# Kernel tuning notes

Hardware: AMD Instinct MI355X
Metric: run time of the kernel (lower is better)

Reference implementation:

```python
import jax, jax.numpy as jnp
import numpy as np

B, S, E, H, I = 32, 257, 1024, 16, 4096
D = E // H  # head_dim = 64
EPS = 1e-5


def setup_inputs() -> dict:
    key = jax.random.key(0)
    ks = jax.random.split(key, 12)
    std = 0.02
    inp = {
        'hidden_states': jax.random.normal(ks[0], (B, S, E), jnp.float32),
        'attention_mask': jnp.zeros((B, 1, S, S), jnp.float32),
        'causal_attention_mask': jnp.zeros((B, 1, S, S), jnp.float32),
        'ln1_w': jnp.ones((E,), jnp.float32),
        'ln1_b': jnp.zeros((E,), jnp.float32),
        'q_w': jax.random.normal(ks[1], (E, E), jnp.float32) * std,
        'q_b': jnp.zeros((E,), jnp.float32),
        'k_w': jax.random.normal(ks[2], (E, E), jnp.float32) * std,
        'k_b': jnp.zeros((E,), jnp.float32),
        'v_w': jax.random.normal(ks[3], (E, E), jnp.float32) * std,
        'v_b': jnp.zeros((E,), jnp.float32),
        'o_w': jax.random.normal(ks[4], (E, E), jnp.float32) * std,
        'o_b': jnp.zeros((E,), jnp.float32),
        'ln2_w': jnp.ones((E,), jnp.float32),
        'ln2_b': jnp.zeros((E,), jnp.float32),
        'fc1_w': jax.random.normal(ks[5], (I, E), jnp.float32) * std,
        'fc1_b': jnp.zeros((I,), jnp.float32),
        'fc2_w': jax.random.normal(ks[6], (E, I), jnp.float32) * std,
        'fc2_b': jnp.zeros((E,), jnp.float32),
    }
    return inp


def _layernorm(x, w, b):
    mu = jnp.mean(x, axis=-1, keepdims=True)
    var = jnp.mean(jnp.square(x - mu), axis=-1, keepdims=True)
    return (x - mu) * jax.lax.rsqrt(var + EPS) * w + b


def _gelu_tanh(x):
    # 0.5*x*(1+tanh(sqrt(2/pi)*(x+0.044715*x^3)))
    c = np.sqrt(2.0 / np.pi).astype(np.float32)
    return 0.5 * x * (1.0 + jnp.tanh(c * (x + 0.044715 * x * x * x)))


def reference(hidden_states, attention_mask, causal_attention_mask,
              ln1_w, ln1_b, q_w, q_b, k_w, k_b, v_w, v_b, o_w, o_b,
              ln2_w, ln2_b, fc1_w, fc1_b, fc2_w, fc2_b):
    scale = D ** -0.5
    residual = hidden_states
    x = _layernorm(hidden_states, ln1_w, ln1_b)

    # projections (torch Linear: x @ W.T + b), q pre-scaled as in source
    q = (x @ q_w.T + q_b) * scale
    k = x @ k_w.T + k_b
    v = x @ v_w.T + v_b

    # [B, H, S, D]
    q = q.reshape(B, S, H, D).transpose(0, 2, 1, 3)
    k = k.reshape(B, S, H, D).transpose(0, 2, 1, 3)
    v = v.reshape(B, S, H, D).transpose(0, 2, 1, 3)

    scores = jnp.einsum('bhqd,bhkd->bhqk', q, k)  # [B,H,S,S]
    scores = scores + causal_attention_mask + attention_mask
    probs = jax.nn.softmax(scores, axis=-1)
    ctx = jnp.einsum('bhqk,bhkd->bhqd', probs, v)
    ctx = ctx.transpose(0, 2, 1, 3).reshape(B, S, E)
    attn_out = ctx @ o_w.T + o_b

    h = residual + attn_out
    residual = h
    x = _layernorm(h, ln2_w, ln2_b)
    x = _gelu_tanh(x @ fc1_w.T + fc1_b)
    x = x @ fc2_w.T + fc2_b
    return residual + x
```

## Files before the change

### kernel.cpp

```cpp
#include <hip/hip_runtime.h>

typedef unsigned short u16;
typedef unsigned int   u32;
typedef short s16x8 __attribute__((ext_vector_type(8)));
typedef float f32x4 __attribute__((ext_vector_type(4)));

#define MFMA16(A,B,C) __builtin_amdgcn_mfma_f32_16x16x32_bf16((A),(B),(C),0,0,0)
#define BAR()  asm volatile("s_barrier" ::: "memory")
#define VMC4   asm volatile("s_waitcnt vmcnt(4)" ::: "memory")
#define VMC0   asm volatile("s_waitcnt vmcnt(0)" ::: "memory")

#define B_   32
#define S_   257
#define E_   1024
#define H_   16
#define D_   64
#define I_   4096
#define M_   (B_*S_)

__device__ __forceinline__ u16 f2bf(float f) {
    u32 u = __float_as_uint(f);
    u32 r = u + 0x7fffu + ((u >> 16) & 1u);
    return (u16)(r >> 16);
}
__device__ __forceinline__ float bf2f(u16 b) {
    return __uint_as_float(((u32)b) << 16);
}

__device__ __forceinline__ void gload16(const void* g, void* l) {
    __builtin_amdgcn_global_load_lds(
        (const __attribute__((address_space(1))) u32*)g,
        (__attribute__((address_space(3))) u32*)l, 16, 0, 0);
}

__global__ __launch_bounds__(256)
void convert_w_kernel(const float* __restrict__ qw, const float* __restrict__ kw,
                      const float* __restrict__ vw, const float* __restrict__ ow,
                      const float* __restrict__ f1, const float* __restrict__ f2,
                      u16* __restrict__ dst)
{
    const int total4 = (12 * 1048576) / 4;
    for (int i = blockIdx.x * 256 + threadIdx.x; i < total4; i += gridDim.x * 256) {
        int e = i * 4;
        int seg = e >> 20;
        const float* srcp; int off;
        if (seg < 4)      { srcp = (seg == 0 ? qw : seg == 1 ? kw : seg == 2 ? vw : ow); off = e & 1048575; }
        else if (seg < 8) { srcp = f1; off = e - 4 * 1048576; }
        else              { srcp = f2; off = e - 8 * 1048576; }
        float4 v = *(const float4*)(srcp + off);
        ushort4 o;
        o.x = f2bf(v.x); o.y = f2bf(v.y); o.z = f2bf(v.z); o.w = f2bf(v.w);
        *(ushort4*)(dst + e) = o;
    }
}

__global__ __launch_bounds__(256)
void mask_combine_kernel(const float* __restrict__ am, const float* __restrict__ cm,
                         u16* __restrict__ msum)
{
    const int total = B_ * S_ * 272;
    for (int i = blockIdx.x * 256 + threadIdx.x; i < total; i += gridDim.x * 256) {
        int skv = i % 272;
        int rem = i / 272;
        int sq  = rem % S_;
        int b   = rem / S_;
        float v;
        if (skv < S_) {
            size_t o = ((size_t)b * S_ + sq) * S_ + skv;
            v = am[o] + cm[o];
        } else v = -1e30f;
        msum[i] = f2bf(v);
    }
}

__global__ __launch_bounds__(256)
void ln_kernel(const float* __restrict__ src, const float* __restrict__ gam,
               const float* __restrict__ bet, u16* __restrict__ dst)
{
    int row = blockIdx.x;
    const float4* p = (const float4*)(src + (size_t)row * E_);
    float4 x = p[threadIdx.x];
    float s  = x.x + x.y + x.z + x.w;
    float s2 = x.x * x.x + x.y * x.y + x.z * x.z + x.w * x.w;
#pragma unroll
    for (int xm = 1; xm < 64; xm <<= 1) {
        s  += __shfl_xor(s,  xm, 64);
        s2 += __shfl_xor(s2, xm, 64);
    }
    __shared__ float red[8];
    int wv = threadIdx.x >> 6;
    if ((threadIdx.x & 63) == 0) { red[wv] = s; red[4 + wv] = s2; }
    __syncthreads();
    s  = red[0] + red[1] + red[2] + red[3];
    s2 = red[4] + red[5] + red[6] + red[7];
    float mu  = s * (1.0f / 1024.0f);
    float var = s2 * (1.0f / 1024.0f) - mu * mu;
    float rs  = rsqrtf(var + 1e-5f);
    float4 g  = ((const float4*)gam)[threadIdx.x];
    float4 be = ((const float4*)bet)[threadIdx.x];
    ushort4 o;
    o.x = f2bf((x.x - mu) * rs * g.x + be.x);
    o.y = f2bf((x.y - mu) * rs * g.y + be.y);
    o.z = f2bf((x.z - mu) * rs * g.z + be.z);
    o.w = f2bf((x.w - mu) * rs * g.w + be.w);
    ((ushort4*)dst)[(size_t)row * 256 + threadIdx.x] = o;
}

template<int MODE>
__global__ __launch_bounds__(256, 3)
void gemm4(const u16* __restrict__ A,
           const u16* __restrict__ Bq, const u16* __restrict__ Bk, const u16* __restrict__ Bv,
           const float* __restrict__ biasq, const float* __restrict__ biask, const float* __restrict__ biasvv,
           const float* __restrict__ res, float* __restrict__ outF,
           u16* __restrict__ outBq, u16* __restrict__ outBk, u16* __restrict__ outBv,
           int M, int N, int K)
{
    __shared__ u16 lds[2][2][4096];
    const int tid = threadIdx.x, lane = tid & 63, w = tid >> 6;
    const int lr = lane & 15, lg = lane >> 4;
    const int wm = w >> 1, wn = w & 1;

    const u16* Bm = Bq; const float* bias = biasq; u16* outB = outBq;
    float scl = 1.0f;
    int nt = blockIdx.y;
    if (MODE == 0) {
        int mat = nt >> 3; nt &= 7;
        if (mat == 1)      { Bm = Bk; bias = biask; outB = outBk; }
        else if (mat == 2) { Bm = Bv; bias = biasvv; outB = outBv; }
        if (mat == 0) scl = 0.125f;
    }
    const int m0 = blockIdx.x * 128, n0 = nt * 128;
    const int NTt = K >> 5;

    const int p    = tid * 16;
    const int l_   = p ^ (((p >> 7) & 3) << 4);
    const int srow = l_ >> 6;
    const int scol = (l_ & 63) >> 1;
    const int wbase = w * 1024;

    auto STAGE = [&](int buf, int t) {
        const int kc = t << 5;
        {   int gr = m0 + srow;       if (gr > M - 1) gr = M - 1;
            gload16(A  + (size_t)gr * K + kc + scol, (char*)&lds[buf][0][0] + wbase); }
        {   int gr = m0 + 64 + srow;  if (gr > M - 1) gr = M - 1;
            gload16(A  + (size_t)gr * K + kc + scol, (char*)&lds[buf][0][0] + 4096 + wbase); }
        {   int gr = n0 + srow;       if (gr > N - 1) gr = N - 1;
            gload16(Bm + (size_t)gr * K + kc + scol, (char*)&lds[buf][1][0] + wbase); }
        {   int gr = n0 + 64 + srow;  if (gr > N - 1) gr = N - 1;
            gload16(Bm + (size_t)gr * K + kc + scol, (char*)&lds[buf][1][0] + 4096 + wbase); }
    };
    auto LDA = [&](int buf, int mf) -> s16x8 {
        const char* b = (const char*)&lds[buf][0][0];
        int row = wm * 64 + mf * 16 + lr;
        return *(const s16x8*)(b + row * 64 + ((lg * 16) ^ (((row >> 1) & 3) << 4)));
    };
    auto LDB = [&](int buf, int nf) -> s16x8 {
        const char* b = (const char*)&lds[buf][1][0];
        int row = wn * 64 + nf * 16 + lr;
        return *(const s16x8*)(b + row * 64 + ((lg * 16) ^ (((row >> 1) & 3) << 4)));
    };

    f32x4 acc[4][4];
#pragma unroll
    for (int i = 0; i < 4; ++i)
#pragma unroll
        for (int j = 0; j < 4; ++j) { f32x4 z = {0.f, 0.f, 0.f, 0.f}; acc[i][j] = z; }

    STAGE(0, 0);
    STAGE(1, 1);
    VMC4;
    BAR();

    for (int t = 0; t < NTt; ++t) {
        const int cur = t & 1;
        s16x8 bf[4], af[4];
#pragma unroll
        for (int nf = 0; nf < 4; ++nf) bf[nf] = LDB(cur, nf);
#pragma unroll
        for (int mf = 0; mf < 4; ++mf) af[mf] = LDA(cur, mf);
#pragma unroll
        for (int mf = 0; mf < 4; ++mf)
#pragma unroll
            for (int nf = 0; nf < 4; ++nf)
                acc[mf][nf] = MFMA16(af[mf], bf[nf], acc[mf][nf]);
        BAR();
        if (t + 2 < NTt) STAGE(cur, t + 2);
        if (t + 1 < NTt) {
            if (t + 2 < NTt) { VMC4; } else { VMC0; }
        }
        BAR();
    }

    float biasv[4];
#pragma unroll
    for (int nf = 0; nf < 4; ++nf)
        biasv[nf] = bias[n0 + wn * 64 + nf * 16 + lr];

#pragma unroll
    for (int mf = 0; mf < 4; ++mf) {
#pragma unroll
        for (int r = 0; r < 4; ++r) {
            int row = m0 + wm * 64 + mf * 16 + lg * 4 + r;
            if (row >= M) continue;
            if (MODE == 0) {
                int bb = row / S_;
                int ss = row - bb * S_;
#pragma unroll
                for (int nf = 0; nf < 4; ++nf) {
                    int col = n0 + wn * 64 + nf * 16 + lr;
                    int hh = col >> 6, dd = col & 63;
                    float v = (acc[mf][nf][r] + biasv[nf]) * scl;
                    outB[(((size_t)bb * H_ + hh) * S_ + ss) * D_ + dd] = f2bf(v);
                }
            } else if (MODE == 1) {
                size_t base = (size_t)row * N;
#pragma unroll
                for (int nf = 0; nf < 4; ++nf) {
                    int col = n0 + wn * 64 + nf * 16 + lr;
                    outF[base + col] = acc[mf][nf][r] + biasv[nf] + res[base + col];
                }
            } else {
                size_t base = (size_t)row * N;
#pragma unroll
                for (int nf = 0; nf < 4; ++nf) {
                    int col = n0 + wn * 64 + nf * 16 + lr;
                    float x = acc[mf][nf][r] + biasv[nf];
                    float u2 = 1.5957691216057308f * (x + 0.044715f * x * x * x);
                    u2 = fminf(u2, 80.0f);
                    float tt = __expf(u2);
                    outB[base + col] = f2bf(x * tt / (1.0f + tt));
                }
            }
        }
    }
}

__global__ __launch_bounds__(256)
void attn_kernel(const u16* __restrict__ qg_, const u16* __restrict__ kg_,
                 const u16* __restrict__ vg_, const u16* __restrict__ msum,
                 u16* __restrict__ ctx)
{
    __shared__ u16 Ks[272 * 72];
    __shared__ u16 Vt[64 * 296];
    __shared__ u16 Ps[4][16 * 32];
    const int bh = blockIdx.x;
    const int b = bh >> 4, hh = bh & 15;
    const u16* kg = kg_ + (size_t)bh * (S_ * D_);
    const u16* vg = vg_ + (size_t)bh * (S_ * D_);
    const u16* qg = qg_ + (size_t)bh * (S_ * D_);
    const int tid = threadIdx.x, lane = tid & 63, wv = tid >> 6;

    for (int c = tid; c < (S_ * D_) / 8; c += 256) {
        int s = c >> 3, d8 = (c & 7) << 3;
        s16x8 val = *(const s16x8*)(kg + s * 64 + d8);
        *(s16x8*)&Ks[s * 72 + d8] = val;
    }
    for (int idx = tid; idx < 15 * 64; idx += 256) {
        int rr = 257 + (idx >> 6), cc = idx & 63;
        Ks[rr * 72 + cc] = 0;
    }
    for (int c = tid; c < (S_ * D_) / 8; c += 256) {
        int s = c >> 3, d8 = (c & 7) << 3;
        s16x8 val = *(const s16x8*)(vg + s * 64 + d8);
#pragma unroll
        for (int j = 0; j < 8; ++j) Vt[(d8 + j) * 296 + s] = (u16)val[j];
    }
    for (int idx = tid; idx < 64 * 39; idx += 256) {
        int dd = idx / 39, cc = 257 + idx % 39;
        Vt[dd * 296 + cc] = 0;
    }
    __syncthreads();

    const int lr = lane & 15, lg = lane >> 4;
    for (int qb = wv; qb < 17; qb += 4) {
        const int q0 = qb * 16;
        int qrow = q0 + lr; if (qrow > S_ - 1) qrow = S_ - 1;
        s16x8 aq0 = *(const s16x8*)(qg + qrow * 64 + lg * 8);
        s16x8 aq1 = *(const s16x8*)(qg + qrow * 64 + 32 + lg * 8);

        f32x4 sc[17];
#pragma unroll
        for (int t = 0; t < 17; ++t) { f32x4 z = {0.f, 0.f, 0.f, 0.f}; sc[t] = z; }
#pragma unroll
        for (int t = 0; t < 17; ++t) {
            s16x8 b0 = *(const s16x8*)&Ks[(t * 16 + lr) * 72 + lg * 8];
            s16x8 b1 = *(const s16x8*)&Ks[(t * 16 + lr) * 72 + 32 + lg * 8];
            sc[t] = MFMA16(aq0, b0, sc[t]);
            sc[t] = MFMA16(aq1, b1, sc[t]);
        }
        float mx[4] = {-3e38f, -3e38f, -3e38f, -3e38f};
#pragma unroll
        for (int r = 0; r < 4; ++r) {
            int sq = q0 + lg * 4 + r; if (sq > S_ - 1) sq = S_ - 1;
            const u16* mrow = msum + ((size_t)b * S_ + sq) * 272;
#pragma unroll
            for (int t = 0; t < 17; ++t) {
                sc[t][r] += bf2f(mrow[t * 16 + lr]);
                mx[r] = fmaxf(mx[r], sc[t][r]);
            }
        }
#pragma unroll
        for (int r = 0; r < 4; ++r) {
#pragma unroll
            for (int xm = 1; xm <= 8; xm <<= 1)
                mx[r] = fmaxf(mx[r], __shfl_xor(mx[r], xm, 64));
        }
        float sum[4] = {0.f, 0.f, 0.f, 0.f};
#pragma unroll
        for (int t = 0; t < 17; ++t)
#pragma unroll
            for (int r = 0; r < 4; ++r) {
                float e = __expf(sc[t][r] - mx[r]);
                sc[t][r] = e; sum[r] += e;
            }
#pragma unroll
        for (int r = 0; r < 4; ++r) {
#pragma unroll
            for (int xm = 1; xm <= 8; xm <<= 1)
                sum[r] += __shfl_xor(sum[r], xm, 64);
        }

        f32x4 ac[4];
#pragma unroll
        for (int nt = 0; nt < 4; ++nt) { f32x4 z = {0.f, 0.f, 0.f, 0.f}; ac[nt] = z; }
        u16* myP = &Ps[wv][0];
#pragma unroll
        for (int kc = 0; kc < 9; ++kc) {
#pragma unroll
            for (int tt = 0; tt < 2; ++tt) {
                const int t = kc * 2 + tt;
#pragma unroll
                for (int r = 0; r < 4; ++r) {
                    float pv = (t < 17) ? sc[(t < 17) ? t : 0][r] : 0.f;
                    myP[(lg * 4 + r) * 32 + tt * 16 + lr] = f2bf(pv);
                }
            }
            s16x8 pa = *(const s16x8*)&myP[lr * 32 + lg * 8];
#pragma unroll
            for (int nt = 0; nt < 4; ++nt) {
                s16x8 bv = *(const s16x8*)&Vt[(nt * 16 + lr) * 296 + kc * 32 + lg * 8];
                ac[nt] = MFMA16(pa, bv, ac[nt]);
            }
        }
#pragma unroll
        for (int r = 0; r < 4; ++r) {
            int sq = q0 + lg * 4 + r;
            if (sq < S_) {
                float rd = 1.0f / sum[r];
                size_t base = (((size_t)b * S_ + sq) * H_ + hh) * D_;
#pragma unroll
                for (int nt = 0; nt < 4; ++nt)
                    ctx[base + nt * 16 + lr] = f2bf(ac[nt][r] * rd);
            }
        }
    }
}

extern "C" void kernel_launch(void* const* d_in, const int* in_sizes, int n_in,
                              void* d_out, int out_size, void* d_ws, size_t ws_size,
                              hipStream_t stream)
{
    const float* hid   = (const float*)d_in[0];
    const float* am    = (const float*)d_in[1];
    const float* cm    = (const float*)d_in[2];
    const float* ln1w  = (const float*)d_in[3];
    const float* ln1b  = (const float*)d_in[4];
    const float* qw    = (const float*)d_in[5];
    const float* qbias = (const float*)d_in[6];
    const float* kw    = (const float*)d_in[7];
    const float* kbias = (const float*)d_in[8];
    const float* vw    = (const float*)d_in[9];
    const float* vbias = (const float*)d_in[10];
    const float* ow    = (const float*)d_in[11];
    const float* obias = (const float*)d_in[12];
    const float* ln2w  = (const float*)d_in[13];
    const float* ln2b  = (const float*)d_in[14];
    const float* f1w   = (const float*)d_in[15];
    const float* f1b   = (const float*)d_in[16];
    const float* f2w   = (const float*)d_in[17];
    const float* f2b   = (const float*)d_in[18];
    float* out = (float*)d_out;

    const size_t ME = (size_t)M_ * E_;
    u16* Wq   = (u16*)d_ws;
    u16* Wk   = Wq + 1048576;
    u16* Wv   = Wk + 1048576;
    u16* Wo   = Wv + 1048576;
    u16* Wf1  = Wo + 1048576;
    u16* Wf2  = Wf1 + 4 * 1048576;
    u16* xln  = Wf2 + 4 * 1048576;
    u16* qb_  = xln + ME;
    u16* kb_  = qb_ + ME;
    u16* vb_  = kb_ + ME;
    u16* ctx  = vb_ + ME;
    float* hbuf = (float*)(ctx + ME);
    u16* msum = (u16*)(hbuf + ME);
    u16* act  = qb_;
    u16* x2   = xln;

    convert_w_kernel<<<3072, 256, 0, stream>>>(qw, kw, vw, ow, f1w, f2w, Wq);
    mask_combine_kernel<<<8736, 256, 0, stream>>>(am, cm, msum);
    ln_kernel<<<M_, 256, 0, stream>>>(hid, ln1w, ln1b, xln);
    gemm4<0><<<dim3(65, 24), 256, 0, stream>>>(xln, Wq, Wk, Wv, qbias, kbias, vbias,
                                               nullptr, nullptr, qb_, kb_, vb_,
                                               M_, 1024, 1024);
    attn_kernel<<<512, 256, 0, stream>>>(qb_, kb_, vb_, msum, ctx);
    gemm4<1><<<dim3(65, 8), 256, 0, stream>>>(ctx, Wo, nullptr, nullptr, obias, nullptr, nullptr,
                                              hid, hbuf, nullptr, nullptr, nullptr,
                                              M_, 1024, 1024);
    ln_kernel<<<M_, 256, 0, stream>>>(hbuf, ln2w, ln2b, x2);
    gemm4<2><<<dim3(65, 32), 256, 0, stream>>>(x2, Wf1, nullptr, nullptr, f1b, nullptr, nullptr,
                                               nullptr, nullptr, act, nullptr, nullptr,
                                               M_, 4096, 1024);
    gemm4<1><<<dim3(65, 8), 256, 0, stream>>>(act, Wf2, nullptr, nullptr, f2b, nullptr, nullptr,
                                              hbuf, out, nullptr, nullptr, nullptr,
                                              M_, 1024, 4096);
}
```

Baseline: 456.6 us.

## Enlarge GEMM tiles to 256x128 and remap workgroups per XCD

```diff
diff --git a/kernel.cpp b/kernel.cpp
--- a/kernel.cpp
+++ b/kernel.cpp
@@ -7,7 +7,7 @@
 
 #define MFMA16(A,B,C) __builtin_amdgcn_mfma_f32_16x16x32_bf16((A),(B),(C),0,0,0)
 #define BAR()  asm volatile("s_barrier" ::: "memory")
-#define VMC4   asm volatile("s_waitcnt vmcnt(4)" ::: "memory")
+#define VMC6   asm volatile("s_waitcnt vmcnt(6)" ::: "memory")
 #define VMC0   asm volatile("s_waitcnt vmcnt(0)" ::: "memory")
 
 #define B_   32
@@ -17,6 +17,7 @@
 #define D_   64
 #define I_   4096
 #define M_   (B_*S_)
+#define MT_  33
 
 __device__ __forceinline__ u16 f2bf(float f) {
     u32 u = __float_as_uint(f);
@@ -107,29 +108,35 @@
 }
 
 template<int MODE>
-__global__ __launch_bounds__(256, 3)
-void gemm4(const u16* __restrict__ A,
+__global__ __launch_bounds__(256, 2)
+void gemmW(const u16* __restrict__ A,
            const u16* __restrict__ Bq, const u16* __restrict__ Bk, const u16* __restrict__ Bv,
            const float* __restrict__ biasq, const float* __restrict__ biask, const float* __restrict__ biasvv,
            const float* __restrict__ res, float* __restrict__ outF,
            u16* __restrict__ outBq, u16* __restrict__ outBk, u16* __restrict__ outBv,
            int M, int N, int K)
 {
-    __shared__ u16 lds[2][2][4096];
+    __shared__ u16 lds[2][6][2048];
     const int tid = threadIdx.x, lane = tid & 63, w = tid >> 6;
     const int lr = lane & 15, lg = lane >> 4;
     const int wm = w >> 1, wn = w & 1;
 
+    const int nwg = gridDim.x;
+    const int q8 = nwg >> 3, r8 = nwg & 7;
+    const int xcd = blockIdx.x & 7, o8 = blockIdx.x >> 3;
+    int wg = (xcd < r8 ? xcd * (q8 + 1) : r8 * (q8 + 1) + (xcd - r8) * q8) + o8;
+
     const u16* Bm = Bq; const float* bias = biasq; u16* outB = outBq;
     float scl = 1.0f;
-    int nt = blockIdx.y;
+    const int NTL = N >> 7;
     if (MODE == 0) {
-        int mat = nt >> 3; nt &= 7;
+        int mat = wg / (MT_ * NTL); wg -= mat * (MT_ * NTL);
         if (mat == 1)      { Bm = Bk; bias = biask; outB = outBk; }
         else if (mat == 2) { Bm = Bv; bias = biasvv; outB = outBv; }
         if (mat == 0) scl = 0.125f;
     }
-    const int m0 = blockIdx.x * 128, n0 = nt * 128;
+    const int mt = wg / NTL, nt = wg - mt * NTL;
+    const int m0 = mt * 256, n0 = nt * 128;
     const int NTt = K >> 5;
 
     const int p    = tid * 16;
@@ -140,53 +147,57 @@
 
     auto STAGE = [&](int buf, int t) {
         const int kc = t << 5;
-        {   int gr = m0 + srow;       if (gr > M - 1) gr = M - 1;
-            gload16(A  + (size_t)gr * K + kc + scol, (char*)&lds[buf][0][0] + wbase); }
-        {   int gr = m0 + 64 + srow;  if (gr > M - 1) gr = M - 1;
-            gload16(A  + (size_t)gr * K + kc + scol, (char*)&lds[buf][0][0] + 4096 + wbase); }
-        {   int gr = n0 + srow;       if (gr > N - 1) gr = N - 1;
-            gload16(Bm + (size_t)gr * K + kc + scol, (char*)&lds[buf][1][0] + wbase); }
-        {   int gr = n0 + 64 + srow;  if (gr > N - 1) gr = N - 1;
-            gload16(Bm + (size_t)gr * K + kc + scol, (char*)&lds[buf][1][0] + 4096 + wbase); }
+#pragma unroll
+        for (int s = 0; s < 4; ++s) {
+            int gr = m0 + s * 64 + srow; if (gr > M - 1) gr = M - 1;
+            gload16(A + (size_t)gr * K + kc + scol, (char*)&lds[buf][s][0] + wbase);
+        }
+#pragma unroll
+        for (int s = 0; s < 2; ++s) {
+            int gr = n0 + s * 64 + srow; if (gr > N - 1) gr = N - 1;
+            gload16(Bm + (size_t)gr * K + kc + scol, (char*)&lds[buf][4 + s][0] + wbase);
+        }
     };
     auto LDA = [&](int buf, int mf) -> s16x8 {
-        const char* b = (const char*)&lds[buf][0][0];
-        int row = wm * 64 + mf * 16 + lr;
-        return *(const s16x8*)(b + row * 64 + ((lg * 16) ^ (((row >> 1) & 3) << 4)));
+        int row = wm * 128 + mf * 16 + lr;
+        const char* b = (const char*)&lds[buf][row >> 6][0];
+        int ir = row & 63;
+        return *(const s16x8*)(b + ir * 64 + ((lg * 16) ^ (((ir >> 1) & 3) << 4)));
     };
     auto LDB = [&](int buf, int nf) -> s16x8 {
-        const char* b = (const char*)&lds[buf][1][0];
         int row = wn * 64 + nf * 16 + lr;
-        return *(const s16x8*)(b + row * 64 + ((lg * 16) ^ (((row >> 1) & 3) << 4)));
+        const char* b = (const char*)&lds[buf][4 + (row >> 6)][0];
+        int ir = row & 63;
+        return *(const s16x8*)(b + ir * 64 + ((lg * 16) ^ (((ir >> 1) & 3) << 4)));
     };
 
-    f32x4 acc[4][4];
-#pragma unroll
-    for (int i = 0; i < 4; ++i)
+    f32x4 acc[8][4];
+#pragma unroll
+    for (int i = 0; i < 8; ++i)
 #pragma unroll
         for (int j = 0; j < 4; ++j) { f32x4 z = {0.f, 0.f, 0.f, 0.f}; acc[i][j] = z; }
 
     STAGE(0, 0);
     STAGE(1, 1);
-    VMC4;
+    VMC6;
     BAR();
 
     for (int t = 0; t < NTt; ++t) {
         const int cur = t & 1;
-        s16x8 bf[4], af[4];
+        s16x8 bf[4];
 #pragma unroll
         for (int nf = 0; nf < 4; ++nf) bf[nf] = LDB(cur, nf);
 #pragma unroll
-        for (int mf = 0; mf < 4; ++mf) af[mf] = LDA(cur, mf);
-#pragma unroll
-        for (int mf = 0; mf < 4; ++mf)
+        for (int mf = 0; mf < 8; ++mf) {
+            s16x8 a = LDA(cur, mf);
 #pragma unroll
             for (int nf = 0; nf < 4; ++nf)
-                acc[mf][nf] = MFMA16(af[mf], bf[nf], acc[mf][nf]);
+                acc[mf][nf] = MFMA16(a, bf[nf], acc[mf][nf]);
+        }
         BAR();
         if (t + 2 < NTt) STAGE(cur, t + 2);
         if (t + 1 < NTt) {
-            if (t + 2 < NTt) { VMC4; } else { VMC0; }
+            if (t + 2 < NTt) { VMC6; } else { VMC0; }
         }
         BAR();
     }
@@ -197,10 +208,10 @@
         biasv[nf] = bias[n0 + wn * 64 + nf * 16 + lr];
 
 #pragma unroll
-    for (int mf = 0; mf < 4; ++mf) {
+    for (int mf = 0; mf < 8; ++mf) {
 #pragma unroll
         for (int r = 0; r < 4; ++r) {
-            int row = m0 + wm * 64 + mf * 16 + lg * 4 + r;
+            int row = m0 + wm * 128 + mf * 16 + lg * 4 + r;
             if (row >= M) continue;
             if (MODE == 0) {
                 int bb = row / S_;
@@ -401,18 +412,18 @@
     convert_w_kernel<<<3072, 256, 0, stream>>>(qw, kw, vw, ow, f1w, f2w, Wq);
     mask_combine_kernel<<<8736, 256, 0, stream>>>(am, cm, msum);
     ln_kernel<<<M_, 256, 0, stream>>>(hid, ln1w, ln1b, xln);
-    gemm4<0><<<dim3(65, 24), 256, 0, stream>>>(xln, Wq, Wk, Wv, qbias, kbias, vbias,
-                                               nullptr, nullptr, qb_, kb_, vb_,
-                                               M_, 1024, 1024);
+    gemmW<0><<<3 * MT_ * 8, 256, 0, stream>>>(xln, Wq, Wk, Wv, qbias, kbias, vbias,
+                                              nullptr, nullptr, qb_, kb_, vb_,
+                                              M_, 1024, 1024);
     attn_kernel<<<512, 256, 0, stream>>>(qb_, kb_, vb_, msum, ctx);
-    gemm4<1><<<dim3(65, 8), 256, 0, stream>>>(ctx, Wo, nullptr, nullptr, obias, nullptr, nullptr,
-                                              hid, hbuf, nullptr, nullptr, nullptr,
-                                              M_, 1024, 1024);
+    gemmW<1><<<MT_ * 8, 256, 0, stream>>>(ctx, Wo, nullptr, nullptr, obias, nullptr, nullptr,
+                                          hid, hbuf, nullptr, nullptr, nullptr,
+                                          M_, 1024, 1024);
     ln_kernel<<<M_, 256, 0, stream>>>(hbuf, ln2w, ln2b, x2);
-    gemm4<2><<<dim3(65, 32), 256, 0, stream>>>(x2, Wf1, nullptr, nullptr, f1b, nullptr, nullptr,
-                                               nullptr, nullptr, act, nullptr, nullptr,
-                                               M_, 4096, 1024);
-    gemm4<1><<<dim3(65, 8), 256, 0, stream>>>(act, Wf2, nullptr, nullptr, f2b, nullptr, nullptr,
-                                              hbuf, out, nullptr, nullptr, nullptr,
-                                              M_, 1024, 4096);
-}
+    gemmW<2><<<MT_ * 32, 256, 0, stream>>>(x2, Wf1, nullptr, nullptr, f1b, nullptr, nullptr,
+                                           nullptr, nullptr, act, nullptr, nullptr,
+                                           M_, 4096, 1024);
+    gemmW<1><<<MT_ * 8, 256, 0, stream>>>(act, Wf2, nullptr, nullptr, f2b, nullptr, nullptr,
+                                          hbuf, out, nullptr, nullptr, nullptr,
+                                          M_, 1024, 4096);
+}
```

Result: faster. 427.6 us (-6.4%).
